# Kernel tuning notes

Measured on AMD Instinct MI355X. Metric: run time of the kernel, lower is better.

## Reference

```python
import jax, jax.numpy as jnp
import numpy as np
from jax import lax

B, CIN, T, H, W_ = 16, 8, 20, 64, 64
COUT = 32
K = 3


def setup_inputs() -> dict:
    key = jax.random.key(0)
    ks = jax.random.split(key, 6)
    scale = 0.05
    return {
        "X": jax.random.normal(ks[0], (B, CIN, T, H, W_), dtype=jnp.float32),
        "W": jax.random.normal(ks[1], (4 * COUT, CIN + COUT, K, K), dtype=jnp.float32) * scale,
        "b": jax.random.normal(ks[2], (4 * COUT,), dtype=jnp.float32) * scale,
        "W_ci": jax.random.normal(ks[3], (COUT, H, W_), dtype=jnp.float32) * scale,
        "W_cf": jax.random.normal(ks[4], (COUT, H, W_), dtype=jnp.float32) * scale,
        "W_co": jax.random.normal(ks[5], (COUT, H, W_), dtype=jnp.float32) * scale,
    }


def reference(X, W, b, W_ci, W_cf, W_co):
    # X: (B, Cin, T, H, W) -> output (B, Cout, T, H, W)
    Bb, Cin, Tt, Hh, Ww = X.shape
    Cout = W_ci.shape[0]

    def conv(x):  # x: (B, Cin+Cout, H, W)
        y = lax.conv_general_dilated(
            x, W, window_strides=(1, 1), padding="SAME",
            dimension_numbers=("NCHW", "OIHW", "NCHW"))
        return y + b[None, :, None, None]

    def step(carry, x_t):
        h, c = carry
        gates = conv(jnp.concatenate([x_t, h], axis=1))  # (B, 4*Cout, H, W)
        i_c, f_c, cc_c, o_c = jnp.split(gates, 4, axis=1)
        i_g = jax.nn.sigmoid(i_c + W_ci[None] * c)
        f_g = jax.nn.sigmoid(f_c + W_cf[None] * c)
        c_new = f_g * c + i_g * jnp.tanh(cc_c)
        o_g = jax.nn.sigmoid(o_c + W_co[None] * c_new)
        h_new = o_g * jnp.tanh(c_new)
        return (h_new, c_new), h_new

    h0 = jnp.zeros((Bb, Cout, Hh, Ww), dtype=X.dtype)
    c0 = jnp.zeros((Bb, Cout, Hh, Ww), dtype=X.dtype)
    x_seq = jnp.moveaxis(X, 2, 0)  # (T, B, Cin, H, W)
    _, hs = lax.scan(step, (h0, c0), x_seq)  # hs: (T, B, Cout, H, W)
    return jnp.moveaxis(hs, 0, 2)  # (B, Cout, T, H, W)
```

## Files before the change

### kernel.cpp

```cpp
#include <hip/hip_runtime.h>
#include <math.h>

#define Bn   16
#define CIN  8
#define NT   20
#define COUT 32
#define HW   4096
#define NTHREADS 256

typedef __attribute__((ext_vector_type(8)))  short bf16x8;
typedef __attribute__((ext_vector_type(16))) float f32x16;
typedef __attribute__((ext_vector_type(4)))  int   int4v;

__device__ inline unsigned short f2bf(float f) {
    unsigned u = __builtin_bit_cast(unsigned, f);
    u += 0x7fffu + ((u >> 16) & 1u);
    return (unsigned short)(u >> 16);
}
__device__ inline float bf2f(unsigned short u) {
    return __builtin_bit_cast(float, (unsigned)u << 16);
}
__device__ inline float sigm(float x) {
    return 1.0f / (1.0f + __expf(-x));
}
__device__ inline float tanh_fast(float x) {
    x = fminf(fmaxf(x, -15.0f), 15.0f);
    float e = __expf(2.0f * x);
    return (e - 1.0f) / (e + 1.0f);
}

__global__ __launch_bounds__(256) void prep_w(const float* __restrict__ W,
                                              unsigned short* __restrict__ Wbf) {
    int idx = blockIdx.x * 256 + threadIdx.x;
    if (idx >= 9 * 3 * 2 * 128 * 8) return;
    int e    = idx & 7;
    int m    = (idx >> 3) & 127;
    int half = (idx >> 10) & 1;
    int fk   = idx >> 11;
    int kb   = fk % 3;
    int tap  = fk / 3;
    int ch   = kb * 16 + half * 8 + e;
    int co   = m >> 2;
    int g    = m & 3;
    float v = 0.0f;
    if (ch < 40) v = W[(size_t)((g * 32 + co) * 40 + ch) * 9 + tap];
    Wbf[idx] = f2bf(v);
}

__global__ __launch_bounds__(256) void zero_flags(int* flags) {
    flags[blockIdx.x * 256 + threadIdx.x] = 0;
}

__global__ __launch_bounds__(NTHREADS, 2) void convlstm_persist(
    const float* __restrict__ X,
    const unsigned short* __restrict__ Wbf,
    const float* __restrict__ bias,
    const float* __restrict__ Wci,
    const float* __restrict__ Wcf,
    const float* __restrict__ Wco,
    float* __restrict__ out,
    unsigned long long* __restrict__ stage,
    int* __restrict__ flags)
{
    __shared__ __align__(16) unsigned char smem[33792 + 24576 + 512];
    unsigned short* Wlds = (unsigned short*)(smem + 33792);
    float*          lds_b = (float*)(smem + 33792 + 24576);

    const int tid = threadIdx.x;
    const int pid = blockIdx.x;
    const int b   = pid >> 5;
    const int TI  = ((pid & 7) << 2) | ((pid >> 3) & 3);
    const int r0  = TI * 2;

    const int wid  = tid >> 6;
    const int lane = tid & 63;
    const int lm   = lane & 31;
    const int half = lane >> 5;

    {
        int4v z = {0, 0, 0, 0};
        for (int i = tid; i < 2112; i += NTHREADS) *(int4v*)(smem + i * 16) = z;
    }
    {
        const float* wsrc[3] = {Wci, Wcf, Wco};
#pragma unroll
        for (int pl = 0; pl < 3; ++pl)
            for (int i = tid; i < 4096; i += NTHREADS) {
                int co = i >> 7, p = i & 127;
                Wlds[pl * 4096 + i] = f2bf(wsrc[pl][(co << 12) + TI * 128 + p]);
            }
        if (tid < 128) lds_b[tid] = bias[tid];
    }

    bf16x8 Af[27];
#pragma unroll
    for (int f = 0; f < 27; ++f)
        Af[f] = *(const bf16x8*)(Wbf + (size_t)((f * 2 + half) * 128 + wid * 32 + lm) * 8);

    float creg[16];
#pragma unroll
    for (int i = 0; i < 16; ++i) creg[i] = 0.0f;

    const unsigned sel0 = half ? 0x01000504u : 0x05040100u;
    const unsigned sel1 = sel0 + 0x02020202u;
    int* myflag = flags + (b << 5) + TI;

    __syncthreads();

    for (int t = 0; t < NT; ++t) {
        if (t > 0) {
            if (tid < 2) {
                const int nti = TI + (tid ? 1 : -1);
                if ((unsigned)nti < 32u) {
                    const int* fp = flags + (b << 5) + nti;
                    while (__hip_atomic_load(fp, __ATOMIC_RELAXED,
                                             __HIP_MEMORY_SCOPE_AGENT) < t)
                        __builtin_amdgcn_s_sleep(2);
                }
            }
            __syncthreads();
        }

        {
            const int  gr    = r0 + wid - 1;
            const bool rok   = (unsigned)gr < 64u;
            const int  lc    = lane + 1;
            const int  cell0 = wid * 33 + (lc >> 1);
            const int  sbase = (lc & 1) << 3;
            const int  sx    = (lc >> 1) & 15;

            if (rok) {
                const float* xp = X + ((((size_t)b * CIN) * NT + t) << 12)
                                    + (gr << 6) + lane;
                const size_t chs = (size_t)NT << 12;
                float x0 = xp[0],       x1 = xp[chs],     x2 = xp[2 * chs], x3 = xp[3 * chs];
                float x4 = xp[4 * chs], x5 = xp[5 * chs], x6 = xp[6 * chs], x7 = xp[7 * chs];
                unsigned d0, d1, d2, d3;
                asm("v_cvt_pk_bf16_f32 %0, %1, %2" : "=v"(d0) : "v"(x0), "v"(x1));
                asm("v_cvt_pk_bf16_f32 %0, %1, %2" : "=v"(d1) : "v"(x2), "v"(x3));
                asm("v_cvt_pk_bf16_f32 %0, %1, %2" : "=v"(d2) : "v"(x4), "v"(x5));
                asm("v_cvt_pk_bf16_f32 %0, %1, %2" : "=v"(d3) : "v"(x6), "v"(x7));
                int4v xq = {(int)d0, (int)d1, (int)d2, (int)d3};
                *(int4v*)(smem + cell0 * 256 + ((sbase ^ sx) << 4)) = xq;
            }
            const bool need_halo =
                (t > 0) && ((wid == 0 && TI > 0) || (wid == 3 && TI < 31));
            if (need_halo) {
                const unsigned long long* sp =
                    stage + ((((size_t)((t - 1) & 1) * Bn + b) * 64 + gr) << 9) + lane;
#pragma unroll
                for (int qq = 0; qq < 4; ++qq) {
                    unsigned long long v0 = __hip_atomic_load(
                        sp + (2 * qq) * 64, __ATOMIC_RELAXED, __HIP_MEMORY_SCOPE_AGENT);
                    unsigned long long v1 = __hip_atomic_load(
                        sp + (2 * qq + 1) * 64, __ATOMIC_RELAXED, __HIP_MEMORY_SCOPE_AGENT);
                    const int slot = (sbase | (qq + 1)) ^ sx;
                    int4v hv = {(int)(unsigned)v0, (int)(v0 >> 32),
                                (int)(unsigned)v1, (int)(v1 >> 32)};
                    *(int4v*)(smem + cell0 * 256 + (slot << 4)) = hv;
                }
            }
        }
        __syncthreads();

        f32x16 acc[4];
#pragma unroll
        for (int nb = 0; nb < 4; ++nb)
#pragma unroll
            for (int r = 0; r < 16; ++r) acc[nb][r] = 0.0f;

        __builtin_amdgcn_s_setprio(1);
#pragma unroll
        for (int dy = 0; dy < 3; ++dy)
#pragma unroll
            for (int dx = 0; dx < 3; ++dx)
#pragma unroll
                for (int kb = 0; kb < 3; ++kb) {
                    const int f    = (dy * 3 + dx) * 3 + kb;
                    const int cidx = kb * 2 + half;
#pragma unroll
                    for (int nb = 0; nb < 4; ++nb) {
                        const int lr   = (nb >> 1) + dy;
                        const int lc   = lm + (nb & 1) * 32 + dx;
                        const int slot = (((lc & 1) << 3) + cidx) ^ ((lc >> 1) & 15);
                        const bf16x8 bf =
                            *(const bf16x8*)(smem + (lr * 33 + (lc >> 1)) * 256 + slot * 16);
                        acc[nb] = __builtin_amdgcn_mfma_f32_32x32x16_bf16(Af[f], bf, acc[nb], 0, 0, 0);
                    }
                }
        __builtin_amdgcn_s_setprio(0);

        __syncthreads();

#pragma unroll
        for (int nb = 0; nb < 4; ++nb) {
            const int p_loc = nb * 32 + lm;
            const int pos   = TI * 128 + p_loc;
            const int col   = (nb & 1) * 32 + lm;
            const int lc    = col + 1;
            const int cell  = (1 + (nb >> 1)) * 33 + (lc >> 1);
            const int sbase = (lc & 1) << 3;
            const int sx    = (lc >> 1) & 15;
            const int row   = r0 + (nb >> 1);
            const bool hstore = (nb >> 1) ? (TI < 31) : (TI > 0);
            float hprev = 0.0f;
#pragma unroll
            for (int j = 0; j < 4; ++j) {
                const int co  = wid * 8 + 2 * j + half;
                const int wof = (co << 7) + p_loc;
                const float c0 = creg[nb * 4 + j];
                const float gi = acc[nb][4 * j + 0] + lds_b[co]      + bf2f(Wlds[wof]) * c0;
                const float gf = acc[nb][4 * j + 1] + lds_b[32 + co] + bf2f(Wlds[4096 + wof]) * c0;
                const float gc = acc[nb][4 * j + 2] + lds_b[64 + co];
                const float gq = acc[nb][4 * j + 3] + lds_b[96 + co];

                const float ig = sigm(gi);
                const float fg = sigm(gf);
                const float cn = fg * c0 + ig * tanh_fast(gc);
                const float og = sigm(gq + bf2f(Wlds[2 * 4096 + wof]) * cn);
                const float hn = og * tanh_fast(cn);

                creg[nb * 4 + j] = cn;
                out[(((size_t)(b * COUT + co) * NT + t) << 12) + pos] = hn;

                if (j & 1) {
                    unsigned pk;
                    asm("v_cvt_pk_bf16_f32 %0, %1, %2" : "=v"(pk) : "v"(hprev), "v"(hn));
                    unsigned other = (unsigned)__shfl_xor((int)pk, 32, 64);
                    unsigned q0 = __builtin_amdgcn_perm(other, pk, sel0);
                    unsigned q1 = __builtin_amdgcn_perm(other, pk, sel1);
                    const int a = j >> 1;
                    if (half == a) {
                        const int q8 = wid * 2 + a;
                        const unsigned long long quad =
                            ((unsigned long long)q1 << 32) | q0;
                        const int tq = 2 + q8;
                        *(unsigned long long*)(smem + cell * 256 +
                            (((sbase | (tq >> 1)) ^ sx) << 4) + ((tq & 1) << 3)) = quad;
                        if (hstore)
                            __hip_atomic_store(
                                stage + ((((size_t)(t & 1) * Bn + b) * 64 + row) << 9)
                                      + (q8 << 6) + col,
                                quad, __ATOMIC_RELAXED, __HIP_MEMORY_SCOPE_AGENT);
                    }
                } else {
                    hprev = hn;
                }
            }
        }

        __syncthreads();
        if (tid == 0)
            __hip_atomic_store(myflag, t + 1, __ATOMIC_RELAXED,
                               __HIP_MEMORY_SCOPE_AGENT);
    }
}

extern "C" void kernel_launch(void* const* d_in, const int* in_sizes, int n_in,
                              void* d_out, int out_size, void* d_ws, size_t ws_size,
                              hipStream_t stream) {
    const float* X    = (const float*)d_in[0];
    const float* Wf   = (const float*)d_in[1];
    const float* bias = (const float*)d_in[2];
    const float* Wci  = (const float*)d_in[3];
    const float* Wcf  = (const float*)d_in[4];
    const float* Wco  = (const float*)d_in[5];
    float* out = (float*)d_out;

    unsigned short*     Wbf   = (unsigned short*)d_ws;
    int*                flags = (int*)((char*)d_ws + 110592);
    unsigned long long* stage = (unsigned long long*)((char*)d_ws + 112640);

    prep_w<<<216, 256, 0, stream>>>(Wf, Wbf);
    zero_flags<<<2, 256, 0, stream>>>(flags);
    convlstm_persist<<<Bn * 32, NTHREADS, 0, stream>>>(
        X, Wbf, bias, Wci, Wcf, Wco, out, stage, flags);
}
```

Before: 327.2 us.

## Prefetch next-step X, keep peephole weights in registers, localize halo waits

Moves the peephole weights and bias out of LDS into per-thread registers and precomputes all LDS/global addresses outside the time loop. The next timestep's X values are loaded into registers right after the barrier so the loads overlap the MFMA work. Neighbour-flag spinning now happens only in the halo-loading wavefronts instead of two threads followed by a block-wide barrier, which removes one barrier per step. It also drops the s_setprio hints. The extra registers (precomputed addresses, weights, prefetch buffer) may add pressure at the two-blocks-per-CU launch bound.

```diff
diff --git a/kernel.cpp b/kernel.cpp
--- a/kernel.cpp
+++ b/kernel.cpp
@@ -16,9 +16,6 @@
     unsigned u = __builtin_bit_cast(unsigned, f);
     u += 0x7fffu + ((u >> 16) & 1u);
     return (unsigned short)(u >> 16);
-}
-__device__ inline float bf2f(unsigned short u) {
-    return __builtin_bit_cast(float, (unsigned)u << 16);
 }
 __device__ inline float sigm(float x) {
     return 1.0f / (1.0f + __expf(-x));
@@ -62,9 +59,7 @@
     unsigned long long* __restrict__ stage,
     int* __restrict__ flags)
 {
-    __shared__ __align__(16) unsigned char smem[33792 + 24576 + 512];
-    unsigned short* Wlds = (unsigned short*)(smem + 33792);
-    float*          lds_b = (float*)(smem + 33792 + 24576);
+    __shared__ __align__(16) unsigned char smem[33792];
 
     const int tid = threadIdx.x;
     const int pid = blockIdx.x;
@@ -81,147 +76,175 @@
         int4v z = {0, 0, 0, 0};
         for (int i = tid; i < 2112; i += NTHREADS) *(int4v*)(smem + i * 16) = z;
     }
-    {
-        const float* wsrc[3] = {Wci, Wcf, Wco};
-#pragma unroll
-        for (int pl = 0; pl < 3; ++pl)
-            for (int i = tid; i < 4096; i += NTHREADS) {
-                int co = i >> 7, p = i & 127;
-                Wlds[pl * 4096 + i] = f2bf(wsrc[pl][(co << 12) + TI * 128 + p]);
-            }
-        if (tid < 128) lds_b[tid] = bias[tid];
-    }
 
     bf16x8 Af[27];
 #pragma unroll
     for (int f = 0; f < 27; ++f)
         Af[f] = *(const bf16x8*)(Wbf + (size_t)((f * 2 + half) * 128 + wid * 32 + lm) * 8);
 
+    float bias_v[4][4];
+    float wci_r[4][4], wcf_r[4][4], wco_r[4][4];
+#pragma unroll
+    for (int j = 0; j < 4; ++j) {
+        const int co = wid * 8 + 2 * j + half;
+#pragma unroll
+        for (int g = 0; g < 4; ++g) bias_v[j][g] = bias[g * 32 + co];
+        const int pofs = (co << 12) + TI * 128 + lm;
+#pragma unroll
+        for (int nb = 0; nb < 4; ++nb) {
+            wci_r[nb][j] = Wci[pofs + nb * 32];
+            wcf_r[nb][j] = Wcf[pofs + nb * 32];
+            wco_r[nb][j] = Wco[pofs + nb * 32];
+        }
+    }
+
+    int dsa[3][3][4];
+#pragma unroll
+    for (int dx = 0; dx < 3; ++dx)
+#pragma unroll
+        for (int kb = 0; kb < 3; ++kb)
+#pragma unroll
+            for (int nb = 0; nb < 4; ++nb) {
+                const int lc   = lm + (nb & 1) * 32 + dx;
+                const int slot = (((lc & 1) << 3) + kb * 2 + half) ^ ((lc >> 1) & 15);
+                dsa[dx][kb][nb] = ((nb >> 1) * 33 + (lc >> 1)) * 256 + slot * 16;
+            }
+    const int  gr   = r0 + wid - 1;
+    const bool rok  = (unsigned)gr < 64u;
+    const int  lcF  = lane + 1;
+    const int  celF = wid * 33 + (lcF >> 1);
+    const int  sbF  = (lcF & 1) << 3;
+    const int  sxF  = (lcF >> 1) & 15;
+    const int  adrX = celF * 256 + (((sbF | 0) ^ sxF) << 4);
+    int adrH[4];
+#pragma unroll
+    for (int qq = 0; qq < 4; ++qq)
+        adrH[qq] = celF * 256 + ((((sbF | (qq + 1)) ^ sxF)) << 4);
+    const int tq = 2 + wid * 2 + half;
+    int adrE[4];
+#pragma unroll
+    for (int nb = 0; nb < 4; ++nb) {
+        const int col = (nb & 1) * 32 + lm;
+        const int lc  = col + 1;
+        const int sb  = (lc & 1) << 3;
+        const int sx  = (lc >> 1) & 15;
+        adrE[nb] = ((1 + (nb >> 1)) * 33 + (lc >> 1)) * 256
+                 + (((sb | (tq >> 1)) ^ sx) << 4) + ((tq & 1) << 3);
+    }
+    float* outp[4];
+#pragma unroll
+    for (int j = 0; j < 4; ++j) {
+        const int co = wid * 8 + 2 * j + half;
+        outp[j] = out + (((size_t)(b * COUT + co) * NT) << 12) + TI * 128 + lm;
+    }
+    const size_t par_off = (size_t)Bn << 15;
+    unsigned long long* stp0 =
+        stage + (((size_t)b * 64 + r0) << 9) + ((wid * 2 + half) << 6) + lm;
+    const unsigned long long* hlp =
+        stage + (((size_t)b * 64 + (rok ? gr : 0)) << 9) + lane;
+    const float*  xbase = X + ((((size_t)b * CIN) * NT) << 12) + ((rok ? gr : 0) << 6) + lane;
+    const size_t  chs   = (size_t)NT << 12;
+    int* myflag = flags + (b << 5) + TI;
+
     float creg[16];
 #pragma unroll
     for (int i = 0; i < 16; ++i) creg[i] = 0.0f;
 
     const unsigned sel0 = half ? 0x01000504u : 0x05040100u;
     const unsigned sel1 = sel0 + 0x02020202u;
-    int* myflag = flags + (b << 5) + TI;
+
+    float xr[8];
+    if (rok) {
+#pragma unroll
+        for (int k = 0; k < 8; ++k) xr[k] = xbase[(size_t)k * chs];
+    }
 
     __syncthreads();
 
     for (int t = 0; t < NT; ++t) {
-        if (t > 0) {
-            if (tid < 2) {
-                const int nti = TI + (tid ? 1 : -1);
-                if ((unsigned)nti < 32u) {
-                    const int* fp = flags + (b << 5) + nti;
-                    while (__hip_atomic_load(fp, __ATOMIC_RELAXED,
-                                             __HIP_MEMORY_SCOPE_AGENT) < t)
-                        __builtin_amdgcn_s_sleep(2);
-                }
-            }
-            __syncthreads();
-        }
-
-        {
-            const int  gr    = r0 + wid - 1;
-            const bool rok   = (unsigned)gr < 64u;
-            const int  lc    = lane + 1;
-            const int  cell0 = wid * 33 + (lc >> 1);
-            const int  sbase = (lc & 1) << 3;
-            const int  sx    = (lc >> 1) & 15;
-
-            if (rok) {
-                const float* xp = X + ((((size_t)b * CIN) * NT + t) << 12)
-                                    + (gr << 6) + lane;
-                const size_t chs = (size_t)NT << 12;
-                float x0 = xp[0],       x1 = xp[chs],     x2 = xp[2 * chs], x3 = xp[3 * chs];
-                float x4 = xp[4 * chs], x5 = xp[5 * chs], x6 = xp[6 * chs], x7 = xp[7 * chs];
-                unsigned d0, d1, d2, d3;
-                asm("v_cvt_pk_bf16_f32 %0, %1, %2" : "=v"(d0) : "v"(x0), "v"(x1));
-                asm("v_cvt_pk_bf16_f32 %0, %1, %2" : "=v"(d1) : "v"(x2), "v"(x3));
-                asm("v_cvt_pk_bf16_f32 %0, %1, %2" : "=v"(d2) : "v"(x4), "v"(x5));
-                asm("v_cvt_pk_bf16_f32 %0, %1, %2" : "=v"(d3) : "v"(x6), "v"(x7));
-                int4v xq = {(int)d0, (int)d1, (int)d2, (int)d3};
-                *(int4v*)(smem + cell0 * 256 + ((sbase ^ sx) << 4)) = xq;
-            }
-            const bool need_halo =
-                (t > 0) && ((wid == 0 && TI > 0) || (wid == 3 && TI < 31));
-            if (need_halo) {
-                const unsigned long long* sp =
-                    stage + ((((size_t)((t - 1) & 1) * Bn + b) * 64 + gr) << 9) + lane;
-#pragma unroll
-                for (int qq = 0; qq < 4; ++qq) {
-                    unsigned long long v0 = __hip_atomic_load(
-                        sp + (2 * qq) * 64, __ATOMIC_RELAXED, __HIP_MEMORY_SCOPE_AGENT);
-                    unsigned long long v1 = __hip_atomic_load(
-                        sp + (2 * qq + 1) * 64, __ATOMIC_RELAXED, __HIP_MEMORY_SCOPE_AGENT);
-                    const int slot = (sbase | (qq + 1)) ^ sx;
-                    int4v hv = {(int)(unsigned)v0, (int)(v0 >> 32),
-                                (int)(unsigned)v1, (int)(v1 >> 32)};
-                    *(int4v*)(smem + cell0 * 256 + (slot << 4)) = hv;
-                }
+        if (rok) {
+            unsigned d0, d1, d2, d3;
+            asm("v_cvt_pk_bf16_f32 %0, %1, %2" : "=v"(d0) : "v"(xr[0]), "v"(xr[1]));
+            asm("v_cvt_pk_bf16_f32 %0, %1, %2" : "=v"(d1) : "v"(xr[2]), "v"(xr[3]));
+            asm("v_cvt_pk_bf16_f32 %0, %1, %2" : "=v"(d2) : "v"(xr[4]), "v"(xr[5]));
+            asm("v_cvt_pk_bf16_f32 %0, %1, %2" : "=v"(d3) : "v"(xr[6]), "v"(xr[7]));
+            int4v xq = {(int)d0, (int)d1, (int)d2, (int)d3};
+            *(int4v*)(smem + adrX) = xq;
+        }
+        const bool haloL = (wid == 0) && (TI > 0);
+        const bool haloR = (wid == 3) && (TI < 31);
+        if ((haloL || haloR) && t > 0) {
+            const int nti = haloL ? TI - 1 : TI + 1;
+            if (lane == 0) {
+                const int* fp = flags + (b << 5) + nti;
+                while (__hip_atomic_load(fp, __ATOMIC_RELAXED,
+                                         __HIP_MEMORY_SCOPE_AGENT) < t)
+                    __builtin_amdgcn_s_sleep(1);
+            }
+            const unsigned long long* sp = hlp + (((t - 1) & 1) ? par_off : 0);
+#pragma unroll
+            for (int qq = 0; qq < 4; ++qq) {
+                unsigned long long v0 = __hip_atomic_load(
+                    sp + (2 * qq) * 64, __ATOMIC_RELAXED, __HIP_MEMORY_SCOPE_AGENT);
+                unsigned long long v1 = __hip_atomic_load(
+                    sp + (2 * qq + 1) * 64, __ATOMIC_RELAXED, __HIP_MEMORY_SCOPE_AGENT);
+                int4v hv = {(int)(unsigned)v0, (int)(v0 >> 32),
+                            (int)(unsigned)v1, (int)(v1 >> 32)};
+                *(int4v*)(smem + adrH[qq]) = hv;
             }
         }
         __syncthreads();
 
+        if (rok && t + 1 < NT) {
+            const float* xp = xbase + ((size_t)(t + 1) << 12);
+#pragma unroll
+            for (int k = 0; k < 8; ++k) xr[k] = xp[(size_t)k * chs];
+        }
+
         f32x16 acc[4];
 #pragma unroll
         for (int nb = 0; nb < 4; ++nb)
 #pragma unroll
             for (int r = 0; r < 16; ++r) acc[nb][r] = 0.0f;
 
-        __builtin_amdgcn_s_setprio(1);
 #pragma unroll
         for (int dy = 0; dy < 3; ++dy)
 #pragma unroll
             for (int dx = 0; dx < 3; ++dx)
 #pragma unroll
                 for (int kb = 0; kb < 3; ++kb) {
-                    const int f    = (dy * 3 + dx) * 3 + kb;
-                    const int cidx = kb * 2 + half;
+                    const int f = (dy * 3 + dx) * 3 + kb;
 #pragma unroll
                     for (int nb = 0; nb < 4; ++nb) {
-                        const int lr   = (nb >> 1) + dy;
-                        const int lc   = lm + (nb & 1) * 32 + dx;
-                        const int slot = (((lc & 1) << 3) + cidx) ^ ((lc >> 1) & 15);
                         const bf16x8 bf =
-                            *(const bf16x8*)(smem + (lr * 33 + (lc >> 1)) * 256 + slot * 16);
+                            *(const bf16x8*)(smem + dsa[dx][kb][nb] + dy * 8448);
                         acc[nb] = __builtin_amdgcn_mfma_f32_32x32x16_bf16(Af[f], bf, acc[nb], 0, 0, 0);
                     }
                 }
-        __builtin_amdgcn_s_setprio(0);
 
         __syncthreads();
 
+        const int tofs = t << 12;
+        unsigned long long* stp = stp0 + ((t & 1) ? par_off : 0);
 #pragma unroll
         for (int nb = 0; nb < 4; ++nb) {
-            const int p_loc = nb * 32 + lm;
-            const int pos   = TI * 128 + p_loc;
-            const int col   = (nb & 1) * 32 + lm;
-            const int lc    = col + 1;
-            const int cell  = (1 + (nb >> 1)) * 33 + (lc >> 1);
-            const int sbase = (lc & 1) << 3;
-            const int sx    = (lc >> 1) & 15;
-            const int row   = r0 + (nb >> 1);
-            const bool hstore = (nb >> 1) ? (TI < 31) : (TI > 0);
             float hprev = 0.0f;
 #pragma unroll
             for (int j = 0; j < 4; ++j) {
-                const int co  = wid * 8 + 2 * j + half;
-                const int wof = (co << 7) + p_loc;
                 const float c0 = creg[nb * 4 + j];
-                const float gi = acc[nb][4 * j + 0] + lds_b[co]      + bf2f(Wlds[wof]) * c0;
-                const float gf = acc[nb][4 * j + 1] + lds_b[32 + co] + bf2f(Wlds[4096 + wof]) * c0;
-                const float gc = acc[nb][4 * j + 2] + lds_b[64 + co];
-                const float gq = acc[nb][4 * j + 3] + lds_b[96 + co];
+                const float gi = acc[nb][4 * j + 0] + bias_v[j][0] + wci_r[nb][j] * c0;
+                const float gf = acc[nb][4 * j + 1] + bias_v[j][1] + wcf_r[nb][j] * c0;
+                const float gc = acc[nb][4 * j + 2] + bias_v[j][2];
+                const float gq = acc[nb][4 * j + 3] + bias_v[j][3];
 
                 const float ig = sigm(gi);
                 const float fg = sigm(gf);
                 const float cn = fg * c0 + ig * tanh_fast(gc);
-                const float og = sigm(gq + bf2f(Wlds[2 * 4096 + wof]) * cn);
+                const float og = sigm(gq + wco_r[nb][j] * cn);
                 const float hn = og * tanh_fast(cn);
 
                 creg[nb * 4 + j] = cn;
-                out[(((size_t)(b * COUT + co) * NT + t) << 12) + pos] = hn;
+                outp[j][tofs + nb * 32] = hn;
 
                 if (j & 1) {
                     unsigned pk;
@@ -229,18 +252,14 @@
                     unsigned other = (unsigned)__shfl_xor((int)pk, 32, 64);
                     unsigned q0 = __builtin_amdgcn_perm(other, pk, sel0);
                     unsigned q1 = __builtin_amdgcn_perm(other, pk, sel1);
-                    const int a = j >> 1;
-                    if (half == a) {
-                        const int q8 = wid * 2 + a;
+                    if (half == (j >> 1)) {
                         const unsigned long long quad =
                             ((unsigned long long)q1 << 32) | q0;
-                        const int tq = 2 + q8;
-                        *(unsigned long long*)(smem + cell * 256 +
-                            (((sbase | (tq >> 1)) ^ sx) << 4) + ((tq & 1) << 3)) = quad;
-                        if (hstore)
+                        *(unsigned long long*)(smem + adrE[nb]) = quad;
+                        const bool hst = (nb >> 1) ? (TI < 31) : (TI > 0);
+                        if (hst)
                             __hip_atomic_store(
-                                stage + ((((size_t)(t & 1) * Bn + b) * 64 + row) << 9)
-                                      + (q8 << 6) + col,
+                                stp + ((nb >> 1) << 9) + ((nb & 1) << 5),
                                 quad, __ATOMIC_RELAXED, __HIP_MEMORY_SCOPE_AGENT);
                     }
                 } else {
```

Measured after the change: 452.8 us. +38.4%, slower.

## Prefetch next-step X into registers and move neighbor flag wait into halo waves

Applied to the files above, without the earlier changes.

Loads of the input frame for step t+1 are issued right after the LDS barrier, so their global latency overlaps the MFMA convolution of step t instead of stalling the start of each step. The inter-block flag spin moves from a block-wide pre-barrier wait to lane 0 of the halo-loading waves only. Other waves can write their X slice into LDS without waiting, which cuts one __syncthreads per step. The cost is extra registers for the prefetched values. The spin within a wave relies on lanes reconverging after the lane-0 loop before the halo loads are issued, which gives the intended ordering.

```diff
diff --git a/kernel.cpp b/kernel.cpp
--- a/kernel.cpp
+++ b/kernel.cpp
@@ -105,63 +105,64 @@
     const unsigned sel1 = sel0 + 0x02020202u;
     int* myflag = flags + (b << 5) + TI;
 
+    const int  gr  = r0 + wid - 1;
+    const bool rok = (unsigned)gr < 64u;
+    const float* xbase = X + ((((size_t)b * CIN) * NT) << 12)
+                           + (((rok ? gr : 0)) << 6) + lane;
+    const size_t chs = (size_t)NT << 12;
+    float xr[8];
+    if (rok) {
+#pragma unroll
+        for (int k = 0; k < 8; ++k) xr[k] = xbase[(size_t)k * chs];
+    }
+
     __syncthreads();
 
     for (int t = 0; t < NT; ++t) {
-        if (t > 0) {
-            if (tid < 2) {
-                const int nti = TI + (tid ? 1 : -1);
-                if ((unsigned)nti < 32u) {
-                    const int* fp = flags + (b << 5) + nti;
-                    while (__hip_atomic_load(fp, __ATOMIC_RELAXED,
-                                             __HIP_MEMORY_SCOPE_AGENT) < t)
-                        __builtin_amdgcn_s_sleep(2);
-                }
-            }
-            __syncthreads();
-        }
-
-        {
-            const int  gr    = r0 + wid - 1;
-            const bool rok   = (unsigned)gr < 64u;
-            const int  lc    = lane + 1;
-            const int  cell0 = wid * 33 + (lc >> 1);
-            const int  sbase = (lc & 1) << 3;
-            const int  sx    = (lc >> 1) & 15;
-
-            if (rok) {
-                const float* xp = X + ((((size_t)b * CIN) * NT + t) << 12)
-                                    + (gr << 6) + lane;
-                const size_t chs = (size_t)NT << 12;
-                float x0 = xp[0],       x1 = xp[chs],     x2 = xp[2 * chs], x3 = xp[3 * chs];
-                float x4 = xp[4 * chs], x5 = xp[5 * chs], x6 = xp[6 * chs], x7 = xp[7 * chs];
-                unsigned d0, d1, d2, d3;
-                asm("v_cvt_pk_bf16_f32 %0, %1, %2" : "=v"(d0) : "v"(x0), "v"(x1));
-                asm("v_cvt_pk_bf16_f32 %0, %1, %2" : "=v"(d1) : "v"(x2), "v"(x3));
-                asm("v_cvt_pk_bf16_f32 %0, %1, %2" : "=v"(d2) : "v"(x4), "v"(x5));
-                asm("v_cvt_pk_bf16_f32 %0, %1, %2" : "=v"(d3) : "v"(x6), "v"(x7));
-                int4v xq = {(int)d0, (int)d1, (int)d2, (int)d3};
-                *(int4v*)(smem + cell0 * 256 + ((sbase ^ sx) << 4)) = xq;
-            }
-            const bool need_halo =
-                (t > 0) && ((wid == 0 && TI > 0) || (wid == 3 && TI < 31));
-            if (need_halo) {
-                const unsigned long long* sp =
-                    stage + ((((size_t)((t - 1) & 1) * Bn + b) * 64 + gr) << 9) + lane;
-#pragma unroll
-                for (int qq = 0; qq < 4; ++qq) {
-                    unsigned long long v0 = __hip_atomic_load(
-                        sp + (2 * qq) * 64, __ATOMIC_RELAXED, __HIP_MEMORY_SCOPE_AGENT);
-                    unsigned long long v1 = __hip_atomic_load(
-                        sp + (2 * qq + 1) * 64, __ATOMIC_RELAXED, __HIP_MEMORY_SCOPE_AGENT);
-                    const int slot = (sbase | (qq + 1)) ^ sx;
-                    int4v hv = {(int)(unsigned)v0, (int)(v0 >> 32),
-                                (int)(unsigned)v1, (int)(v1 >> 32)};
-                    *(int4v*)(smem + cell0 * 256 + (slot << 4)) = hv;
-                }
+        const int lcF  = lane + 1;
+        const int celF = wid * 33 + (lcF >> 1);
+        const int sbF  = (lcF & 1) << 3;
+        const int sxF  = (lcF >> 1) & 15;
+        if (rok) {
+            unsigned d0, d1, d2, d3;
+            asm("v_cvt_pk_bf16_f32 %0, %1, %2" : "=v"(d0) : "v"(xr[0]), "v"(xr[1]));
+            asm("v_cvt_pk_bf16_f32 %0, %1, %2" : "=v"(d1) : "v"(xr[2]), "v"(xr[3]));
+            asm("v_cvt_pk_bf16_f32 %0, %1, %2" : "=v"(d2) : "v"(xr[4]), "v"(xr[5]));
+            asm("v_cvt_pk_bf16_f32 %0, %1, %2" : "=v"(d3) : "v"(xr[6]), "v"(xr[7]));
+            int4v xq = {(int)d0, (int)d1, (int)d2, (int)d3};
+            *(int4v*)(smem + celF * 256 + ((sbF ^ sxF) << 4)) = xq;
+        }
+        const bool haloL = (wid == 0) && (TI > 0);
+        const bool haloR = (wid == 3) && (TI < 31);
+        if ((haloL || haloR) && t > 0) {
+            if (lane == 0) {
+                const int nti = haloL ? TI - 1 : TI + 1;
+                const int* fp = flags + (b << 5) + nti;
+                while (__hip_atomic_load(fp, __ATOMIC_RELAXED,
+                                         __HIP_MEMORY_SCOPE_AGENT) < t)
+                    __builtin_amdgcn_s_sleep(1);
+            }
+            const unsigned long long* sp =
+                stage + ((((size_t)((t - 1) & 1) * Bn + b) * 64 + gr) << 9) + lane;
+#pragma unroll
+            for (int qq = 0; qq < 4; ++qq) {
+                unsigned long long v0 = __hip_atomic_load(
+                    sp + (2 * qq) * 64, __ATOMIC_RELAXED, __HIP_MEMORY_SCOPE_AGENT);
+                unsigned long long v1 = __hip_atomic_load(
+                    sp + (2 * qq + 1) * 64, __ATOMIC_RELAXED, __HIP_MEMORY_SCOPE_AGENT);
+                const int slot = (sbF | (qq + 1)) ^ sxF;
+                int4v hv = {(int)(unsigned)v0, (int)(v0 >> 32),
+                            (int)(unsigned)v1, (int)(v1 >> 32)};
+                *(int4v*)(smem + celF * 256 + (slot << 4)) = hv;
             }
         }
         __syncthreads();
+
+        if (rok && t + 1 < NT) {
+            const float* xp = xbase + ((size_t)(t + 1) << 12);
+#pragma unroll
+            for (int k = 0; k < 8; ++k) xr[k] = xp[(size_t)k * chs];
+        }
 
         f32x16 acc[4];
 #pragma unroll
```

Result: slower. 357.1 us (+9.1%).

## Prefetch next-step X into LDS asynchronously and pack peephole weights

Applied to the files above, without the earlier changes.

Issues global_load_lds for the next timestep's input rows right after the MFMA phase, so the X fetch overlaps the gate epilogue and the neighbour wait instead of sitting on the critical path at the start of each step. The three peephole weight planes are packed into one 64-bit LDS word per position, which turns three LDS reads into one. The spin-wait sleep is also shortened. LDS use per block grows, which may limit occupancy, and correctness depends on the async LDS loads having completed before the next step reads them.

```diff
diff --git a/kernel.cpp b/kernel.cpp
--- a/kernel.cpp
+++ b/kernel.cpp
@@ -7,6 +7,11 @@
 #define COUT 32
 #define HW   4096
 #define NTHREADS 256
+
+#define WPK_OFF  33792
+#define XS_OFF   66560
+#define BIAS_OFF 74752
+#define SMEM_SZ  75264
 
 typedef __attribute__((ext_vector_type(8)))  short bf16x8;
 typedef __attribute__((ext_vector_type(16))) float f32x16;
@@ -62,9 +67,9 @@
     unsigned long long* __restrict__ stage,
     int* __restrict__ flags)
 {
-    __shared__ __align__(16) unsigned char smem[33792 + 24576 + 512];
-    unsigned short* Wlds = (unsigned short*)(smem + 33792);
-    float*          lds_b = (float*)(smem + 33792 + 24576);
+    __shared__ __align__(16) unsigned char smem[SMEM_SZ];
+    unsigned long long* Wpk  = (unsigned long long*)(smem + WPK_OFF);
+    float*              lds_b = (float*)(smem + BIAS_OFF);
 
     const int tid = threadIdx.x;
     const int pid = blockIdx.x;
@@ -81,16 +86,15 @@
         int4v z = {0, 0, 0, 0};
         for (int i = tid; i < 2112; i += NTHREADS) *(int4v*)(smem + i * 16) = z;
     }
-    {
-        const float* wsrc[3] = {Wci, Wcf, Wco};
-#pragma unroll
-        for (int pl = 0; pl < 3; ++pl)
-            for (int i = tid; i < 4096; i += NTHREADS) {
-                int co = i >> 7, p = i & 127;
-                Wlds[pl * 4096 + i] = f2bf(wsrc[pl][(co << 12) + TI * 128 + p]);
-            }
-        if (tid < 128) lds_b[tid] = bias[tid];
+    for (int i = tid; i < 4096; i += NTHREADS) {
+        int co = i >> 7, p = i & 127;
+        int g  = (co << 12) + TI * 128 + p;
+        unsigned long long v = (unsigned long long)f2bf(Wci[g])
+                             | ((unsigned long long)f2bf(Wcf[g]) << 16)
+                             | ((unsigned long long)f2bf(Wco[g]) << 32);
+        Wpk[i] = v;
     }
+    if (tid < 128) lds_b[tid] = bias[tid];
 
     bf16x8 Af[27];
 #pragma unroll
@@ -104,6 +108,22 @@
     const unsigned sel0 = half ? 0x01000504u : 0x05040100u;
     const unsigned sel1 = sel0 + 0x02020202u;
     int* myflag = flags + (b << 5) + TI;
+
+    const int  gr   = r0 + wid - 1;
+    const bool rok  = (unsigned)gr < 64u;
+    const float* xbase = X + ((((size_t)b * CIN) * NT) << 12)
+                           + (((rok ? gr : 0)) << 6) + lane;
+    const size_t chs = (size_t)NT << 12;
+    unsigned int* xs_dst = (unsigned int*)(smem + XS_OFF + wid * 2048);
+    const float*  xs_src = (const float*)(smem + XS_OFF + wid * 2048);
+
+    if (rok) {
+#pragma unroll
+        for (int ch = 0; ch < 8; ++ch)
+            __builtin_amdgcn_global_load_lds(
+                (const unsigned int*)(xbase + (size_t)ch * chs),
+                xs_dst + ch * 64, 4, 0, 0);
+    }
 
     __syncthreads();
 
@@ -115,50 +135,44 @@
                     const int* fp = flags + (b << 5) + nti;
                     while (__hip_atomic_load(fp, __ATOMIC_RELAXED,
                                              __HIP_MEMORY_SCOPE_AGENT) < t)
-                        __builtin_amdgcn_s_sleep(2);
+                        __builtin_amdgcn_s_sleep(1);
                 }
             }
             __syncthreads();
         }
 
-        {
-            const int  gr    = r0 + wid - 1;
-            const bool rok   = (unsigned)gr < 64u;
-            const int  lc    = lane + 1;
-            const int  cell0 = wid * 33 + (lc >> 1);
-            const int  sbase = (lc & 1) << 3;
-            const int  sx    = (lc >> 1) & 15;
-
-            if (rok) {
-                const float* xp = X + ((((size_t)b * CIN) * NT + t) << 12)
-                                    + (gr << 6) + lane;
-                const size_t chs = (size_t)NT << 12;
-                float x0 = xp[0],       x1 = xp[chs],     x2 = xp[2 * chs], x3 = xp[3 * chs];
-                float x4 = xp[4 * chs], x5 = xp[5 * chs], x6 = xp[6 * chs], x7 = xp[7 * chs];
-                unsigned d0, d1, d2, d3;
-                asm("v_cvt_pk_bf16_f32 %0, %1, %2" : "=v"(d0) : "v"(x0), "v"(x1));
-                asm("v_cvt_pk_bf16_f32 %0, %1, %2" : "=v"(d1) : "v"(x2), "v"(x3));
-                asm("v_cvt_pk_bf16_f32 %0, %1, %2" : "=v"(d2) : "v"(x4), "v"(x5));
-                asm("v_cvt_pk_bf16_f32 %0, %1, %2" : "=v"(d3) : "v"(x6), "v"(x7));
-                int4v xq = {(int)d0, (int)d1, (int)d2, (int)d3};
-                *(int4v*)(smem + cell0 * 256 + ((sbase ^ sx) << 4)) = xq;
-            }
-            const bool need_halo =
-                (t > 0) && ((wid == 0 && TI > 0) || (wid == 3 && TI < 31));
-            if (need_halo) {
-                const unsigned long long* sp =
-                    stage + ((((size_t)((t - 1) & 1) * Bn + b) * 64 + gr) << 9) + lane;
-#pragma unroll
-                for (int qq = 0; qq < 4; ++qq) {
-                    unsigned long long v0 = __hip_atomic_load(
-                        sp + (2 * qq) * 64, __ATOMIC_RELAXED, __HIP_MEMORY_SCOPE_AGENT);
-                    unsigned long long v1 = __hip_atomic_load(
-                        sp + (2 * qq + 1) * 64, __ATOMIC_RELAXED, __HIP_MEMORY_SCOPE_AGENT);
-                    const int slot = (sbase | (qq + 1)) ^ sx;
-                    int4v hv = {(int)(unsigned)v0, (int)(v0 >> 32),
-                                (int)(unsigned)v1, (int)(v1 >> 32)};
-                    *(int4v*)(smem + cell0 * 256 + (slot << 4)) = hv;
-                }
+        const int lcF  = lane + 1;
+        const int celF = wid * 33 + (lcF >> 1);
+        const int sbF  = (lcF & 1) << 3;
+        const int sxF  = (lcF >> 1) & 15;
+        if (rok) {
+            float x0 = xs_src[0 * 64 + lane], x1 = xs_src[1 * 64 + lane];
+            float x2 = xs_src[2 * 64 + lane], x3 = xs_src[3 * 64 + lane];
+            float x4 = xs_src[4 * 64 + lane], x5 = xs_src[5 * 64 + lane];
+            float x6 = xs_src[6 * 64 + lane], x7 = xs_src[7 * 64 + lane];
+            unsigned d0, d1, d2, d3;
+            asm("v_cvt_pk_bf16_f32 %0, %1, %2" : "=v"(d0) : "v"(x0), "v"(x1));
+            asm("v_cvt_pk_bf16_f32 %0, %1, %2" : "=v"(d1) : "v"(x2), "v"(x3));
+            asm("v_cvt_pk_bf16_f32 %0, %1, %2" : "=v"(d2) : "v"(x4), "v"(x5));
+            asm("v_cvt_pk_bf16_f32 %0, %1, %2" : "=v"(d3) : "v"(x6), "v"(x7));
+            int4v xq = {(int)d0, (int)d1, (int)d2, (int)d3};
+            *(int4v*)(smem + celF * 256 + ((sbF ^ sxF) << 4)) = xq;
+        }
+        const bool need_halo =
+            (t > 0) && ((wid == 0 && TI > 0) || (wid == 3 && TI < 31));
+        if (need_halo) {
+            const unsigned long long* sp =
+                stage + ((((size_t)((t - 1) & 1) * Bn + b) * 64 + gr) << 9) + lane;
+#pragma unroll
+            for (int qq = 0; qq < 4; ++qq) {
+                unsigned long long v0 = __hip_atomic_load(
+                    sp + (2 * qq) * 64, __ATOMIC_RELAXED, __HIP_MEMORY_SCOPE_AGENT);
+                unsigned long long v1 = __hip_atomic_load(
+                    sp + (2 * qq + 1) * 64, __ATOMIC_RELAXED, __HIP_MEMORY_SCOPE_AGENT);
+                const int slot = (sbF | (qq + 1)) ^ sxF;
+                int4v hv = {(int)(unsigned)v0, (int)(v0 >> 32),
+                            (int)(unsigned)v1, (int)(v1 >> 32)};
+                *(int4v*)(smem + celF * 256 + (slot << 4)) = hv;
             }
         }
         __syncthreads();
@@ -191,6 +205,15 @@
         __builtin_amdgcn_s_setprio(0);
 
         __syncthreads();
+
+        if (rok && (t + 1 < NT)) {
+            const float* xp = xbase + ((size_t)(t + 1) << 12);
+#pragma unroll
+            for (int ch = 0; ch < 8; ++ch)
+                __builtin_amdgcn_global_load_lds(
+                    (const unsigned int*)(xp + (size_t)ch * chs),
+                    xs_dst + ch * 64, 4, 0, 0);
+        }
 
 #pragma unroll
         for (int nb = 0; nb < 4; ++nb) {
@@ -207,17 +230,21 @@
 #pragma unroll
             for (int j = 0; j < 4; ++j) {
                 const int co  = wid * 8 + 2 * j + half;
-                const int wof = (co << 7) + p_loc;
+                const unsigned long long wp = Wpk[(co << 7) + p_loc];
+                const float wci = bf2f((unsigned short)wp);
+                const float wcf = bf2f((unsigned short)(wp >> 16));
+                const float wco = bf2f((unsigned short)(wp >> 32));
+
                 const float c0 = creg[nb * 4 + j];
-                const float gi = acc[nb][4 * j + 0] + lds_b[co]      + bf2f(Wlds[wof]) * c0;
-                const float gf = acc[nb][4 * j + 1] + lds_b[32 + co] + bf2f(Wlds[4096 + wof]) * c0;
+                const float gi = acc[nb][4 * j + 0] + lds_b[co]      + wci * c0;
+                const float gf = acc[nb][4 * j + 1] + lds_b[32 + co] + wcf * c0;
                 const float gc = acc[nb][4 * j + 2] + lds_b[64 + co];
                 const float gq = acc[nb][4 * j + 3] + lds_b[96 + co];
 
                 const float ig = sigm(gi);
                 const float fg = sigm(gf);
                 const float cn = fg * c0 + ig * tanh_fast(gc);
-                const float og = sigm(gq + bf2f(Wlds[2 * 4096 + wof]) * cn);
+                const float og = sigm(gq + wco * cn);
                 const float hn = og * tanh_fast(cn);
 
                 creg[nb * 4 + j] = cn;
```

New measurement: 339.1 us. +3.6%, slower.
